# Kernel optimization log

Hardware: AMD Instinct MI355X
Metric: run time of the kernel (lower is better)

Reference implementation:

```python
import jax, jax.numpy as jnp
import numpy as np

N = 10000   # num_nodes
F = 64      # latent_dim
U = 128     # num_units
B = 8       # batch
K = 2       # gcn_step
E = 160000  # edges (avg degree 16)
M = 2 * K + 1  # num_matrices = len(supports)*gcn_step + 1


def setup_inputs() -> dict:
    rng = np.random.default_rng(0)
    rows = rng.integers(0, N, E).astype(np.int32)
    cols = rng.integers(0, N, E).astype(np.int32)
    vals = (rng.random(E).astype(np.float32) + 0.1)
    # random-walk normalization D^{-1} A, per the original utils.calculate_random_walk_matrix
    deg_out = np.zeros(N, np.float32); np.add.at(deg_out, rows, vals)
    deg_in = np.zeros(N, np.float32); np.add.at(deg_in, cols, vals)
    # support1 = (D_out^{-1} A)^T : out[c] += vals/d_out[r] * x[r]  -> dst=cols, src=rows
    w1 = vals / np.maximum(deg_out[rows], 1e-8)
    # support2 = (D_in^{-1} A^T)^T : out[r] += vals/d_in[c] * x[c]  -> dst=rows, src=cols
    w2 = vals / np.maximum(deg_in[cols], 1e-8)

    key = jax.random.key(0)
    ks = jax.random.split(key, 4)

    def xavier(k, shape):
        std = (2.0 / (shape[0] + shape[1])) ** 0.5
        return jax.random.normal(k, shape, jnp.float32) * std

    return {
        'y': jax.random.normal(ks[0], (B, N * F), jnp.float32),
        'W_lat': xavier(ks[1], (M * F, F)),
        'b_lat': jnp.ones((F,), jnp.float32),   # bias_start=1.0, shared (keyed by length)
        'W_units': xavier(ks[2], (M * F, U)),
        'b_units': jnp.zeros((U,), jnp.float32),
        'W_final': xavier(ks[3], (M * U, F)),
        'sup1_w': jnp.asarray(w1),
        'sup2_w': jnp.asarray(w2),
        'edge_rows': jnp.asarray(rows),
        'edge_cols': jnp.asarray(cols),
    }


def _spmm(dst, src, w, x):
    # sparse matmul S @ x with S given as COO edge list; x: (N, Fin, B)
    return jax.ops.segment_sum(w[:, None, None] * x[src], dst, num_segments=N)


def _gconv(x, supports, W, b):
    # x: (B, N, Fin) -> (B, N*Fout); Chebyshev diffusion convolution
    Bsz, n, fin = x.shape
    x0 = jnp.transpose(x, (1, 2, 0))  # (N, Fin, B)
    xs = [x0]
    for dst, src, w in supports:
        xk_2 = x0
        x1 = _spmm(dst, src, w, x0)
        xs.append(x1)
        for _ in range(2, K + 1):
            x2 = 2.0 * _spmm(dst, src, w, x1) - xk_2
            xs.append(x2)
            xk_2, x1 = x1, x2
    X = jnp.stack(xs, axis=-1)                       # (N, Fin, B, M)
    X = jnp.transpose(X, (2, 0, 1, 3)).reshape(Bsz * n, fin * len(xs))  # feature-major, matrix-minor
    out = X @ W + b
    return out.reshape(Bsz, n * W.shape[1])


def reference(y, W_lat, b_lat, W_units, b_units, W_final, sup1_w, sup2_w, edge_rows, edge_cols):
    supports = [(edge_cols, edge_rows, sup1_w), (edge_rows, edge_cols, sup2_w)]
    x = y.reshape(B, N, F)
    # theta gate (bias_start=1.0 via shared b_lat)
    theta = jax.nn.sigmoid(_gconv(x, supports, W_lat, b_lat))
    # ode_func_net: gen_layers=1 hidden gconv + final gconv (final bias is shared b_lat!)
    c = jnp.tanh(_gconv(x, supports, W_units, b_units)).reshape(B, N, U)
    c = jnp.tanh(_gconv(c, supports, W_final, b_lat))
    return -theta * c
```

## Files before the change

### kernel.cpp

```cpp
#include <hip/hip_runtime.h>

#define N_NODES 10000
#define NEDGE 160000
#define NB 80000

typedef unsigned int u32;
typedef unsigned short u16;
typedef __attribute__((ext_vector_type(8))) short short8;
typedef __attribute__((ext_vector_type(4))) float float4v;

__device__ __forceinline__ u16 f2bf(float f) {
    u32 u = __float_as_uint(f);
    return (u16)((u + 0x7fffu + ((u >> 16) & 1u)) >> 16);
}
__device__ __forceinline__ float lo16(u32 u) { return __uint_as_float(u << 16); }
__device__ __forceinline__ float hi16(u32 u) { return __uint_as_float(u & 0xffff0000u); }
__device__ __forceinline__ u32 pack2(float a, float b) {
    return (u32)f2bf(a) | (((u32)f2bf(b)) << 16);
}
__device__ __forceinline__ float fast_tanh(float v) {
    return 1.f - 2.f / (__expf(2.f * v) + 1.f);
}

static const size_t SLAB = (size_t)NB * 64;

__global__ __launch_bounds__(256) void prepcount_kernel(
    const float2* __restrict__ y, u32* __restrict__ X0,
    const float* __restrict__ W_lat, const float* __restrict__ W_units,
    u16* __restrict__ bpk12, const float* __restrict__ W_final, u16* __restrict__ bpkP,
    const int* __restrict__ rows, const int* __restrict__ cols, int* __restrict__ cnt) {
    int b = blockIdx.x, t = threadIdx.x;
    if (b < 10000) {
        int idx = b * 256 + t;
        int fh = idx & 31;
        int rb = idx >> 5;
        int bb = rb & 7;
        int n = rb >> 3;
        float2 v = y[((size_t)bb * N_NODES + n) * 32 + fh];
        X0[idx] = pack2(v.x, v.y);
    } else if (b < 10240) {
        int idx = (b - 10000) * 256 + t;
        int j = idx & 7;
        int lane = (idx >> 3) & 63;
        int rest = idx >> 9;
        int ct = rest % 12;
        int ks = rest / 12;
        int k = ks * 32 + (lane >> 4) * 8 + j;
        int col = ct * 16 + (lane & 15);
        int wrow = (k % 64) * 5 + (k / 64);
        float v = (col < 64) ? W_lat[wrow * 64 + col] : W_units[wrow * 128 + (col - 64)];
        bpk12[idx] = f2bf(v);
    } else if (b < 10400) {
        int idx = (b - 10240) * 256 + t;
        int j8 = idx & 7;
        int lane = (idx >> 3) & 63;
        int rest = idx >> 9;
        int ct = rest % 20;
        int ks = rest / 20;
        int k = ks * 32 + (lane >> 4) * 8 + j8;
        int col = ct * 16 + (lane & 15);
        int slot = col >> 6, j = col & 63;
        float v;
        if (slot == 0)
            v = W_final[(k * 5 + 0) * 64 + j] - W_final[(k * 5 + 2) * 64 + j] -
                W_final[(k * 5 + 4) * 64 + j];
        else
            v = W_final[(k * 5 + slot) * 64 + j];
        bpkP[idx] = f2bf(v);
    } else {
        int e = (b - 10400) * 256 + t;
        atomicAdd(&cnt[cols[e]], 1);
        atomicAdd(&cnt[N_NODES + rows[e]], 1);
    }
}

__global__ void blocksum_kernel(const int* __restrict__ cnt, int* __restrict__ bsums) {
    __shared__ int red[4];
    int arr = blockIdx.x / 40;
    int c = blockIdx.x % 40;
    int idx = c * 256 + threadIdx.x;
    int v = (idx < N_NODES) ? cnt[arr * N_NODES + idx] : 0;
#pragma unroll
    for (int off = 32; off; off >>= 1) v += __shfl_down(v, off, 64);
    int wv = threadIdx.x >> 6, ln = threadIdx.x & 63;
    if (ln == 0) red[wv] = v;
    __syncthreads();
    if (threadIdx.x == 0) bsums[blockIdx.x] = red[0] + red[1] + red[2] + red[3];
}

__global__ void scanapply_kernel(int* __restrict__ cnt, const int* __restrict__ bsums,
                                 int* __restrict__ rowptr1, int* __restrict__ rowptr2) {
    __shared__ int lds[256];
    int arr = blockIdx.x / 40;
    int c = blockIdx.x % 40;
    int base = 0;
    for (int i = 0; i < c; i++) base += bsums[arr * 40 + i];
    int idx = c * 256 + threadIdx.x;
    bool ok = idx < N_NODES;
    int v = ok ? cnt[arr * N_NODES + idx] : 0;
    int t = threadIdx.x;
    lds[t] = v;
    __syncthreads();
    for (int off = 1; off < 256; off <<= 1) {
        int add = (t >= off) ? lds[t - off] : 0;
        __syncthreads();
        lds[t] += add;
        __syncthreads();
    }
    int excl = lds[t] - v + base;
    if (ok) {
        int* rp = arr ? rowptr2 : rowptr1;
        rp[idx] = excl;
        cnt[arr * N_NODES + idx] = excl;
    }
    if (blockIdx.x == 0 && t == 0) {
        rowptr1[N_NODES] = NEDGE;
        rowptr2[N_NODES] = NEDGE;
    }
}

__global__ void scatter_kernel(const int* __restrict__ rows, const int* __restrict__ cols,
                               const float* __restrict__ w1, const float* __restrict__ w2,
                               int* __restrict__ cur1, int* __restrict__ cur2,
                               int2* __restrict__ edges1, int2* __restrict__ edges2) {
    int e = blockIdx.x * 256 + threadIdx.x;
    if (e < NEDGE) {
        int r = rows[e], c = cols[e];
        int p1 = atomicAdd(&cur1[c], 1);
        edges1[p1] = make_int2(r, __float_as_int(w1[e]));
        int p2 = atomicAdd(&cur2[r], 1);
        edges2[p2] = make_int2(c, __float_as_int(w2[e]));
    }
}

__device__ __forceinline__ void gacc(float* acc, float w, uint4 u) {
    acc[0] += w * lo16(u.x); acc[1] += w * hi16(u.x);
    acc[2] += w * lo16(u.y); acc[3] += w * hi16(u.y);
    acc[4] += w * lo16(u.z); acc[5] += w * hi16(u.z);
    acc[6] += w * lo16(u.w); acc[7] += w * hi16(u.w);
}

__device__ __forceinline__ void gather_row(const u32* __restrict__ Xin,
                                           const int* __restrict__ rp,
                                           const int2* __restrict__ eg,
                                           int n, int lane, float* acc) {
    int e0 = rp[n], e1 = rp[n + 1];
    for (int base = e0; base < e1; base += 64) {
        int m = min(64, e1 - base);
        int2 me = make_int2(0, 0);
        if (lane < m) me = eg[base + lane];
        int j = 0;
        for (; j + 8 <= m; j += 8) {
            int s[8];
            float w[8];
            uint4 u[8];
#pragma unroll
            for (int q = 0; q < 8; q++) {
                s[q] = __shfl(me.x, j + q, 64);
                w[q] = __int_as_float(__shfl(me.y, j + q, 64));
            }
#pragma unroll
            for (int q = 0; q < 8; q++)
                u[q] = *(const uint4*)(Xin + (size_t)s[q] * 256 + lane * 4);
#pragma unroll
            for (int q = 0; q < 8; q++) gacc(acc, w[q], u[q]);
        }
        for (; j < m; j++) {
            int src = __shfl(me.x, j, 64);
            float w = __int_as_float(__shfl(me.y, j, 64));
            uint4 u = *(const uint4*)(Xin + (size_t)src * 256 + lane * 4);
            gacc(acc, w, u);
        }
    }
}

__global__ __launch_bounds__(256) void spmm2_kernel(
    const u32* __restrict__ XinA, const u32* __restrict__ XprevA, u32* __restrict__ XoutA,
    const u32* __restrict__ XinB, const u32* __restrict__ XprevB, u32* __restrict__ XoutB,
    const int* __restrict__ rowptr1, const int2* __restrict__ edges1,
    const int* __restrict__ rowptr2, const int2* __restrict__ edges2,
    float alpha, float beta) {
    int lane = threadIdx.x & 63;
    int v = blockIdx.x * 4 + (threadIdx.x >> 6);
    if (v >= 2 * N_NODES) return;
    bool hB = v >= N_NODES;
    int n = hB ? v - N_NODES : v;
    const u32* Xin = hB ? XinB : XinA;
    const u32* Xprev = hB ? XprevB : XprevA;
    u32* Xout = hB ? XoutB : XoutA;
    const int* rp = hB ? rowptr2 : rowptr1;
    const int2* eg = hB ? edges2 : edges1;

    float acc[8] = {0.f, 0.f, 0.f, 0.f, 0.f, 0.f, 0.f, 0.f};
    gather_row(Xin, rp, eg, n, lane, acc);

    size_t o = (size_t)n * 256 + lane * 4;
    if (beta != 0.f) {
        uint4 p = *(const uint4*)(Xprev + o);
        acc[0] = alpha * acc[0] + beta * lo16(p.x); acc[1] = alpha * acc[1] + beta * hi16(p.x);
        acc[2] = alpha * acc[2] + beta * lo16(p.y); acc[3] = alpha * acc[3] + beta * hi16(p.y);
        acc[4] = alpha * acc[4] + beta * lo16(p.z); acc[5] = alpha * acc[5] + beta * hi16(p.z);
        acc[6] = alpha * acc[6] + beta * lo16(p.w); acc[7] = alpha * acc[7] + beta * hi16(p.w);
    } else {
#pragma unroll
        for (int i = 0; i < 8; i++) acc[i] *= alpha;
    }
    uint4 r;
    r.x = pack2(acc[0], acc[1]);
    r.y = pack2(acc[2], acc[3]);
    r.z = pack2(acc[4], acc[5]);
    r.w = pack2(acc[6], acc[7]);
    *(uint4*)(Xout + o) = r;
}

__global__ __launch_bounds__(256) void spmm_final_kernel(
    const u32* __restrict__ T1, const u32* __restrict__ T2,
    const u32* __restrict__ Q, const u32* __restrict__ theta,
    const int* __restrict__ rowptr1, const int2* __restrict__ edges1,
    const int* __restrict__ rowptr2, const int2* __restrict__ edges2,
    float* __restrict__ outF) {
    int lane = threadIdx.x & 63;
    int n = blockIdx.x * 4 + (threadIdx.x >> 6);
    if (n >= N_NODES) return;

    float acc[8] = {0.f, 0.f, 0.f, 0.f, 0.f, 0.f, 0.f, 0.f};
    gather_row(T1, rowptr1, edges1, n, lane, acc);
    gather_row(T2, rowptr2, edges2, n, lane, acc);

    size_t o = (size_t)n * 256 + lane * 4;
    uint4 q = *(const uint4*)(Q + o);
    uint4 th = *(const uint4*)(theta + o);
    float res[8];
    res[0] = -lo16(th.x) * fast_tanh(lo16(q.x) + acc[0]);
    res[1] = -hi16(th.x) * fast_tanh(hi16(q.x) + acc[1]);
    res[2] = -lo16(th.y) * fast_tanh(lo16(q.y) + acc[2]);
    res[3] = -hi16(th.y) * fast_tanh(hi16(q.y) + acc[3]);
    res[4] = -lo16(th.z) * fast_tanh(lo16(q.z) + acc[4]);
    res[5] = -hi16(th.z) * fast_tanh(hi16(q.z) + acc[5]);
    res[6] = -lo16(th.w) * fast_tanh(lo16(q.w) + acc[6]);
    res[7] = -hi16(th.w) * fast_tanh(hi16(q.w) + acc[7]);
    int b = lane >> 3;
    int f0 = ((lane * 4) & 31) * 2;
    float* dst = outF + (size_t)b * (N_NODES * 64) + (size_t)n * 64 + f0;
    *(float4*)(dst) = make_float4(res[0], res[1], res[2], res[3]);
    *(float4*)(dst + 4) = make_float4(res[4], res[5], res[6], res[7]);
}

struct Slabs { const u16* p[5]; };

__global__ __launch_bounds__(256) void gemm12P_kernel(
    Slabs A, const u16* __restrict__ Bp12, const u16* __restrict__ BpP,
    const float* __restrict__ b_lat, const float* __restrict__ b_units,
    u16* __restrict__ theta, u16* __restrict__ P) {
    __shared__ __align__(16) u16 hls[4][16][136];
    int lane = threadIdx.x & 63;
    int wave = threadIdx.x >> 6;
    int rowBase = blockIdx.x * 64 + wave * 16;
    int mrow = lane & 15;
    int kq = lane >> 4;

    float4v acc[12];
#pragma unroll
    for (int c = 0; c < 12; c++) acc[c] = (float4v){0.f, 0.f, 0.f, 0.f};
#pragma unroll
    for (int ks = 0; ks < 10; ks++) {
        int k = ks * 32 + kq * 8;
        int m = k >> 6;
        int koff = k & 63;
        short8 a = *(const short8*)(A.p[m] + (size_t)(rowBase + mrow) * 64 + koff);
        short8 b[12];
#pragma unroll
        for (int ct = 0; ct < 12; ct++)
            b[ct] = *(const short8*)(Bp12 + ((size_t)(ks * 12 + ct) * 64 + lane) * 8);
#pragma unroll
        for (int ct = 0; ct < 12; ct++)
            acc[ct] = __builtin_amdgcn_mfma_f32_16x16x32_bf16(a, b[ct], acc[ct], 0, 0, 0);
    }
#pragma unroll
    for (int ct = 0; ct < 12; ct++) {
        int col = ct * 16 + mrow;
        float bsv = (col < 64) ? b_lat[col] : b_units[col - 64];
#pragma unroll
        for (int i = 0; i < 4; i++) {
            float v = acc[ct][i] + bsv;
            int lr = kq * 4 + i;
            if (col < 64) {
                v = 1.f / (1.f + __expf(-v));
                theta[(size_t)(rowBase + lr) * 64 + col] = f2bf(v);
            } else {
                hls[wave][lr][col - 64] = f2bf(fast_tanh(v));
            }
        }
    }
    __syncthreads();

#pragma unroll
    for (int ch = 0; ch < 2; ch++) {
        float4v pacc[10];
#pragma unroll
        for (int c = 0; c < 10; c++) pacc[c] = (float4v){0.f, 0.f, 0.f, 0.f};
#pragma unroll
        for (int ks = 0; ks < 4; ks++) {
            short8 a = *(const short8*)(&hls[wave][mrow][ks * 32 + kq * 8]);
            short8 b[10];
#pragma unroll
            for (int ct = 0; ct < 10; ct++)
                b[ct] = *(const short8*)(BpP + ((size_t)((ks * 20 + ch * 10 + ct) * 64 + lane)) * 8);
#pragma unroll
            for (int ct = 0; ct < 10; ct++)
                pacc[ct] = __builtin_amdgcn_mfma_f32_16x16x32_bf16(a, b[ct], pacc[ct], 0, 0, 0);
        }
#pragma unroll
        for (int ct = 0; ct < 10; ct++) {
            int col = (ch * 10 + ct) * 16 + mrow;
            float bsv = (col < 64) ? b_lat[col] : 0.f;
#pragma unroll
            for (int i = 0; i < 4; i++) {
                float v = pacc[ct][i] + bsv;
                int r = rowBase + kq * 4 + i;
                P[(size_t)(col >> 6) * SLAB + (size_t)r * 64 + (col & 63)] = f2bf(v);
            }
        }
    }
}

extern "C" void kernel_launch(void* const* d_in, const int* in_sizes, int n_in,
                              void* d_out, int out_size, void* d_ws, size_t ws_size,
                              hipStream_t stream) {
    const float2* y    = (const float2*)d_in[0];
    const float* W_lat = (const float*)d_in[1];
    const float* b_lat = (const float*)d_in[2];
    const float* W_units = (const float*)d_in[3];
    const float* b_units = (const float*)d_in[4];
    const float* W_final = (const float*)d_in[5];
    const float* sup1w = (const float*)d_in[6];
    const float* sup2w = (const float*)d_in[7];
    const int* rows    = (const int*)d_in[8];
    const int* cols    = (const int*)d_in[9];
    float* out = (float*)d_out;

    char* ws = (char*)d_ws;
    size_t off = 0;
    auto alloc = [&](size_t bytes) -> void* {
        void* p = ws + off;
        off += (bytes + 511) & ~(size_t)511;
        return p;
    };
    int* rowptr1 = (int*)alloc((N_NODES + 1) * 4);
    int* rowptr2 = (int*)alloc((N_NODES + 1) * 4);
    int* cnt = (int*)alloc((size_t)2 * N_NODES * 4);
    int* bsums = (int*)alloc(80 * 4);
    int2* edges1 = (int2*)alloc((size_t)NEDGE * 8);
    int2* edges2 = (int2*)alloc((size_t)NEDGE * 8);
    u16* bpk12 = (u16*)alloc((size_t)61440 * 2);
    u16* bpkP = (u16*)alloc((size_t)40960 * 2);
    u16* theta = (u16*)alloc((size_t)NB * 64 * 2);
    u16* S = (u16*)alloc((size_t)5 * NB * 64 * 2);
    u16* P = (u16*)alloc((size_t)5 * NB * 64 * 2);
    u16* T1 = (u16*)alloc((size_t)NB * 64 * 2);
    u16* T2 = (u16*)alloc((size_t)NB * 64 * 2);

    hipMemsetAsync(cnt, 0, (size_t)2 * N_NODES * 4, stream);
    prepcount_kernel<<<11025, 256, 0, stream>>>(y, (u32*)S, W_lat, W_units, bpk12,
                                                W_final, bpkP, rows, cols, cnt);
    blocksum_kernel<<<80, 256, 0, stream>>>(cnt, bsums);
    scanapply_kernel<<<80, 256, 0, stream>>>(cnt, bsums, rowptr1, rowptr2);
    scatter_kernel<<<625, 256, 0, stream>>>(rows, cols, sup1w, sup2w,
                                            cnt, cnt + N_NODES, edges1, edges2);

    const u32* S0 = (const u32*)S;
    u32* X1 = (u32*)(S + 1 * SLAB);
    u32* X2 = (u32*)(S + 2 * SLAB);
    u32* X3 = (u32*)(S + 3 * SLAB);
    u32* X4 = (u32*)(S + 4 * SLAB);
    spmm2_kernel<<<5000, 256, 0, stream>>>(S0, nullptr, X1, S0, nullptr, X3,
                                           rowptr1, edges1, rowptr2, edges2, 1.f, 0.f);
    spmm2_kernel<<<5000, 256, 0, stream>>>(X1, S0, X2, X3, S0, X4,
                                           rowptr1, edges1, rowptr2, edges2, 2.f, -1.f);

    Slabs SX;
    for (int m = 0; m < 5; m++) SX.p[m] = S + (size_t)m * SLAB;
    gemm12P_kernel<<<1250, 256, 0, stream>>>(SX, bpk12, bpkP, b_lat, b_units, theta, P);

    const u32* Q  = (const u32*)(P + 0 * SLAB);
    const u32* P1 = (const u32*)(P + 1 * SLAB);
    const u32* P2 = (const u32*)(P + 2 * SLAB);
    const u32* P3 = (const u32*)(P + 3 * SLAB);
    const u32* P4 = (const u32*)(P + 4 * SLAB);
    spmm2_kernel<<<5000, 256, 0, stream>>>(P2, P1, (u32*)T1, P4, P3, (u32*)T2,
                                           rowptr1, edges1, rowptr2, edges2, 2.f, 1.f);
    spmm_final_kernel<<<2500, 256, 0, stream>>>((const u32*)T1, (const u32*)T2, Q,
                                                (const u32*)theta,
                                                rowptr1, edges1, rowptr2, edges2, out);
}
```

Baseline: 347.5 us.

## Split fused GEMM into two kernels with column-split waves and fuse scan passes

The block-sum and scan-apply kernels become one scan kernel. Each block now recomputes its prefix base by summing the earlier counts, and the running cursors move to a separate buffer. The fused gemm12P kernel is split into gemm12 and gemmP, which pass the hidden activations H0 through global memory. In each new GEMM kernel every wave covers all 64 rows of the block and a slice of the output columns, so each B fragment is reused across four A row tiles and the B loads per wave shrink. This removes one launch in the scan but adds one launch and an extra global write and read of H0 between the GEMMs.

```diff
diff --git a/kernel.cpp b/kernel.cpp
--- a/kernel.cpp
+++ b/kernel.cpp
@@ -74,31 +74,25 @@
     }
 }
 
-__global__ void blocksum_kernel(const int* __restrict__ cnt, int* __restrict__ bsums) {
-    __shared__ int red[4];
-    int arr = blockIdx.x / 40;
-    int c = blockIdx.x % 40;
-    int idx = c * 256 + threadIdx.x;
-    int v = (idx < N_NODES) ? cnt[arr * N_NODES + idx] : 0;
-#pragma unroll
-    for (int off = 32; off; off >>= 1) v += __shfl_down(v, off, 64);
-    int wv = threadIdx.x >> 6, ln = threadIdx.x & 63;
-    if (ln == 0) red[wv] = v;
-    __syncthreads();
-    if (threadIdx.x == 0) bsums[blockIdx.x] = red[0] + red[1] + red[2] + red[3];
-}
-
-__global__ void scanapply_kernel(int* __restrict__ cnt, const int* __restrict__ bsums,
+__global__ void scanfused_kernel(const int* __restrict__ cnt, int* __restrict__ cur,
                                  int* __restrict__ rowptr1, int* __restrict__ rowptr2) {
     __shared__ int lds[256];
     int arr = blockIdx.x / 40;
     int c = blockIdx.x % 40;
-    int base = 0;
-    for (int i = 0; i < c; i++) base += bsums[arr * 40 + i];
-    int idx = c * 256 + threadIdx.x;
+    int t = threadIdx.x;
+    int partial = 0;
+    for (int i = t; i < c * 256; i += 256) partial += cnt[arr * N_NODES + i];
+    lds[t] = partial;
+    __syncthreads();
+    for (int off = 128; off; off >>= 1) {
+        if (t < off) lds[t] += lds[t + off];
+        __syncthreads();
+    }
+    int base = lds[0];
+    __syncthreads();
+    int idx = c * 256 + t;
     bool ok = idx < N_NODES;
     int v = ok ? cnt[arr * N_NODES + idx] : 0;
-    int t = threadIdx.x;
     lds[t] = v;
     __syncthreads();
     for (int off = 1; off < 256; off <<= 1) {
@@ -111,7 +105,7 @@
     if (ok) {
         int* rp = arr ? rowptr2 : rowptr1;
         rp[idx] = excl;
-        cnt[arr * N_NODES + idx] = excl;
+        cur[arr * N_NODES + idx] = excl;
     }
     if (blockIdx.x == 0 && t == 0) {
         rowptr1[N_NODES] = NEDGE;
@@ -248,76 +242,113 @@
 
 struct Slabs { const u16* p[5]; };
 
-__global__ __launch_bounds__(256) void gemm12P_kernel(
-    Slabs A, const u16* __restrict__ Bp12, const u16* __restrict__ BpP,
-    const float* __restrict__ b_lat, const float* __restrict__ b_units,
-    u16* __restrict__ theta, u16* __restrict__ P) {
-    __shared__ __align__(16) u16 hls[4][16][136];
+__global__ __launch_bounds__(256) void gemm12_kernel(
+    Slabs A, const u16* __restrict__ Bp, const float* __restrict__ b_lat,
+    const float* __restrict__ b_units, u16* __restrict__ theta, u16* __restrict__ H0) {
     int lane = threadIdx.x & 63;
     int wave = threadIdx.x >> 6;
-    int rowBase = blockIdx.x * 64 + wave * 16;
+    int rowBase = blockIdx.x * 64;
     int mrow = lane & 15;
     int kq = lane >> 4;
 
-    float4v acc[12];
-#pragma unroll
-    for (int c = 0; c < 12; c++) acc[c] = (float4v){0.f, 0.f, 0.f, 0.f};
+    float4v acc[4][3];
+#pragma unroll
+    for (int s = 0; s < 4; s++)
+#pragma unroll
+        for (int c = 0; c < 3; c++) acc[s][c] = (float4v){0.f, 0.f, 0.f, 0.f};
+
 #pragma unroll
     for (int ks = 0; ks < 10; ks++) {
         int k = ks * 32 + kq * 8;
         int m = k >> 6;
         int koff = k & 63;
-        short8 a = *(const short8*)(A.p[m] + (size_t)(rowBase + mrow) * 64 + koff);
-        short8 b[12];
-#pragma unroll
-        for (int ct = 0; ct < 12; ct++)
-            b[ct] = *(const short8*)(Bp12 + ((size_t)(ks * 12 + ct) * 64 + lane) * 8);
-#pragma unroll
-        for (int ct = 0; ct < 12; ct++)
-            acc[ct] = __builtin_amdgcn_mfma_f32_16x16x32_bf16(a, b[ct], acc[ct], 0, 0, 0);
-    }
-#pragma unroll
-    for (int ct = 0; ct < 12; ct++) {
-        int col = ct * 16 + mrow;
-        float bsv = (col < 64) ? b_lat[col] : b_units[col - 64];
-#pragma unroll
-        for (int i = 0; i < 4; i++) {
-            float v = acc[ct][i] + bsv;
-            int lr = kq * 4 + i;
-            if (col < 64) {
-                v = 1.f / (1.f + __expf(-v));
-                theta[(size_t)(rowBase + lr) * 64 + col] = f2bf(v);
-            } else {
-                hls[wave][lr][col - 64] = f2bf(fast_tanh(v));
+        const u16* abase = A.p[m] + (size_t)(rowBase + mrow) * 64 + koff;
+        short8 a0 = *(const short8*)(abase);
+        short8 a1 = *(const short8*)(abase + 16 * 64);
+        short8 a2 = *(const short8*)(abase + 32 * 64);
+        short8 a3 = *(const short8*)(abase + 48 * 64);
+        short8 b[3];
+#pragma unroll
+        for (int ct = 0; ct < 3; ct++)
+            b[ct] = *(const short8*)(Bp + ((size_t)(ks * 12 + wave * 3 + ct) * 64 + lane) * 8);
+#pragma unroll
+        for (int ct = 0; ct < 3; ct++) {
+            acc[0][ct] = __builtin_amdgcn_mfma_f32_16x16x32_bf16(a0, b[ct], acc[0][ct], 0, 0, 0);
+            acc[1][ct] = __builtin_amdgcn_mfma_f32_16x16x32_bf16(a1, b[ct], acc[1][ct], 0, 0, 0);
+            acc[2][ct] = __builtin_amdgcn_mfma_f32_16x16x32_bf16(a2, b[ct], acc[2][ct], 0, 0, 0);
+            acc[3][ct] = __builtin_amdgcn_mfma_f32_16x16x32_bf16(a3, b[ct], acc[3][ct], 0, 0, 0);
+        }
+    }
+
+#pragma unroll
+    for (int sub = 0; sub < 4; sub++) {
+        int rowq = rowBase + sub * 16 + kq * 4;
+#pragma unroll
+        for (int ct = 0; ct < 3; ct++) {
+            int col = (wave * 3 + ct) * 16 + mrow;
+            float bsv = (col < 64) ? b_lat[col] : b_units[col - 64];
+#pragma unroll
+            for (int i = 0; i < 4; i++) {
+                float v = acc[sub][ct][i] + bsv;
+                int r = rowq + i;
+                if (col < 64) {
+                    v = 1.f / (1.f + __expf(-v));
+                    theta[(size_t)r * 64 + col] = f2bf(v);
+                } else {
+                    H0[(size_t)r * 128 + (col - 64)] = f2bf(fast_tanh(v));
+                }
             }
         }
     }
-    __syncthreads();
-
-#pragma unroll
-    for (int ch = 0; ch < 2; ch++) {
-        float4v pacc[10];
-#pragma unroll
-        for (int c = 0; c < 10; c++) pacc[c] = (float4v){0.f, 0.f, 0.f, 0.f};
-#pragma unroll
-        for (int ks = 0; ks < 4; ks++) {
-            short8 a = *(const short8*)(&hls[wave][mrow][ks * 32 + kq * 8]);
-            short8 b[10];
-#pragma unroll
-            for (int ct = 0; ct < 10; ct++)
-                b[ct] = *(const short8*)(BpP + ((size_t)((ks * 20 + ch * 10 + ct) * 64 + lane)) * 8);
-#pragma unroll
-            for (int ct = 0; ct < 10; ct++)
-                pacc[ct] = __builtin_amdgcn_mfma_f32_16x16x32_bf16(a, b[ct], pacc[ct], 0, 0, 0);
-        }
-#pragma unroll
-        for (int ct = 0; ct < 10; ct++) {
-            int col = (ch * 10 + ct) * 16 + mrow;
+}
+
+__global__ __launch_bounds__(256) void gemmP_kernel(
+    const u16* __restrict__ H0, const u16* __restrict__ Bp,
+    const float* __restrict__ b_lat, u16* __restrict__ P) {
+    int lane = threadIdx.x & 63;
+    int wave = threadIdx.x >> 6;
+    int rowBase = blockIdx.x * 64;
+    int mrow = lane & 15;
+    int kq = lane >> 4;
+
+    float4v acc[4][5];
+#pragma unroll
+    for (int s = 0; s < 4; s++)
+#pragma unroll
+        for (int c = 0; c < 5; c++) acc[s][c] = (float4v){0.f, 0.f, 0.f, 0.f};
+
+#pragma unroll
+    for (int ks = 0; ks < 4; ks++) {
+        int k = ks * 32 + kq * 8;
+        const u16* abase = H0 + (size_t)(rowBase + mrow) * 128 + k;
+        short8 a0 = *(const short8*)(abase);
+        short8 a1 = *(const short8*)(abase + 16 * 128);
+        short8 a2 = *(const short8*)(abase + 32 * 128);
+        short8 a3 = *(const short8*)(abase + 48 * 128);
+        short8 b[5];
+#pragma unroll
+        for (int ct = 0; ct < 5; ct++)
+            b[ct] = *(const short8*)(Bp + ((size_t)(ks * 20 + wave * 5 + ct) * 64 + lane) * 8);
+#pragma unroll
+        for (int ct = 0; ct < 5; ct++) {
+            acc[0][ct] = __builtin_amdgcn_mfma_f32_16x16x32_bf16(a0, b[ct], acc[0][ct], 0, 0, 0);
+            acc[1][ct] = __builtin_amdgcn_mfma_f32_16x16x32_bf16(a1, b[ct], acc[1][ct], 0, 0, 0);
+            acc[2][ct] = __builtin_amdgcn_mfma_f32_16x16x32_bf16(a2, b[ct], acc[2][ct], 0, 0, 0);
+            acc[3][ct] = __builtin_amdgcn_mfma_f32_16x16x32_bf16(a3, b[ct], acc[3][ct], 0, 0, 0);
+        }
+    }
+
+#pragma unroll
+    for (int sub = 0; sub < 4; sub++) {
+        int rowq = rowBase + sub * 16 + kq * 4;
+#pragma unroll
+        for (int ct = 0; ct < 5; ct++) {
+            int col = (wave * 5 + ct) * 16 + mrow;
             float bsv = (col < 64) ? b_lat[col] : 0.f;
 #pragma unroll
             for (int i = 0; i < 4; i++) {
-                float v = pacc[ct][i] + bsv;
-                int r = rowBase + kq * 4 + i;
+                float v = acc[sub][ct][i] + bsv;
+                int r = rowq + i;
                 P[(size_t)(col >> 6) * SLAB + (size_t)r * 64 + (col & 63)] = f2bf(v);
             }
         }
@@ -349,7 +380,7 @@
     int* rowptr1 = (int*)alloc((N_NODES + 1) * 4);
     int* rowptr2 = (int*)alloc((N_NODES + 1) * 4);
     int* cnt = (int*)alloc((size_t)2 * N_NODES * 4);
-    int* bsums = (int*)alloc(80 * 4);
+    int* cur = (int*)alloc((size_t)2 * N_NODES * 4);
     int2* edges1 = (int2*)alloc((size_t)NEDGE * 8);
     int2* edges2 = (int2*)alloc((size_t)NEDGE * 8);
     u16* bpk12 = (u16*)alloc((size_t)61440 * 2);
@@ -357,16 +388,16 @@
     u16* theta = (u16*)alloc((size_t)NB * 64 * 2);
     u16* S = (u16*)alloc((size_t)5 * NB * 64 * 2);
     u16* P = (u16*)alloc((size_t)5 * NB * 64 * 2);
+    u16* H0 = (u16*)alloc((size_t)NB * 128 * 2);
     u16* T1 = (u16*)alloc((size_t)NB * 64 * 2);
     u16* T2 = (u16*)alloc((size_t)NB * 64 * 2);
 
     hipMemsetAsync(cnt, 0, (size_t)2 * N_NODES * 4, stream);
     prepcount_kernel<<<11025, 256, 0, stream>>>(y, (u32*)S, W_lat, W_units, bpk12,
                                                 W_final, bpkP, rows, cols, cnt);
-    blocksum_kernel<<<80, 256, 0, stream>>>(cnt, bsums);
-    scanapply_kernel<<<80, 256, 0, stream>>>(cnt, bsums, rowptr1, rowptr2);
+    scanfused_kernel<<<80, 256, 0, stream>>>(cnt, cur, rowptr1, rowptr2);
     scatter_kernel<<<625, 256, 0, stream>>>(rows, cols, sup1w, sup2w,
-                                            cnt, cnt + N_NODES, edges1, edges2);
+                                            cur, cur + N_NODES, edges1, edges2);
 
     const u32* S0 = (const u32*)S;
     u32* X1 = (u32*)(S + 1 * SLAB);
@@ -380,7 +411,8 @@
 
     Slabs SX;
     for (int m = 0; m < 5; m++) SX.p[m] = S + (size_t)m * SLAB;
-    gemm12P_kernel<<<1250, 256, 0, stream>>>(SX, bpk12, bpkP, b_lat, b_units, theta, P);
+    gemm12_kernel<<<1250, 256, 0, stream>>>(SX, bpk12, b_lat, b_units, theta, H0);
+    gemmP_kernel<<<1250, 256, 0, stream>>>(H0, bpkP, b_lat, P);
 
     const u32* Q  = (const u32*)(P + 0 * SLAB);
     const u32* P1 = (const u32*)(P + 1 * SLAB);
```

Result: slower. 365.8 us (+5.3%).
